# Optimization experiments

Measured on AMD Instinct MI355X. Metric: run time of the kernel, lower is better.

Reference implementation:

```python
import jax, jax.numpy as jnp
import numpy as np

# Module config (from init_kwargs): Occ3D-nuScenes volume
VOL_MIN = np.array([-40.0, -40.0, -1.0], dtype=np.float32)
VOXEL_SIZE = 0.4
GRID_SHAPE = (200, 200, 16)  # (vol_max - vol_min) / voxel_size
K = 6          # fixed per-gaussian window; covers radii <= 0.6m (bbox span <= 5 voxels)
N_GAUSS = 32768
N_DIMS = 16


def setup_inputs() -> dict:
    key = jax.random.key(0)
    k1, k2, k3, k4, k5 = jax.random.split(key, 5)
    # Means strictly inside the volume with 1m margin so bboxes stay in-grid.
    lo = jnp.array([-39.0, -39.0, 0.0], dtype=jnp.float32)
    hi = jnp.array([39.0, 39.0, 4.4], dtype=jnp.float32)
    means3d = jax.random.uniform(k1, (N_GAUSS, 3), minval=lo, maxval=hi, dtype=jnp.float32)
    # SPD covariances: Q diag(s) Q^T with eigenvalues in [0.01, 0.04]
    A = jax.random.normal(k2, (N_GAUSS, 3, 3), dtype=jnp.float32)
    Q, _ = jnp.linalg.qr(A)
    s = jax.random.uniform(k3, (N_GAUSS, 3), minval=0.01, maxval=0.04, dtype=jnp.float32)
    covs = jnp.einsum('nij,nj,nkj->nik', Q, s, Q)
    opacities = jax.random.uniform(k4, (N_GAUSS,), dtype=jnp.float32)
    features = jax.random.normal(k5, (N_GAUSS, N_DIMS), dtype=jnp.float32)
    return {"means3d": means3d, "covs": covs, "opacities": opacities, "features": features}


def reference(means3d, covs, opacities, features):
    N, D = features.shape
    dim_x, dim_y, dim_z = GRID_SHAPE
    total = dim_x * dim_y * dim_z
    vol_min = jnp.asarray(VOL_MIN)

    inv_covs = jnp.linalg.inv(covs)                                  # [N,3,3]
    radii = 3.0 * jnp.sqrt(jnp.diagonal(covs, axis1=-2, axis2=-1))   # [N,3]

    # Bounding box in voxel indices (trunc toward zero, like the triton .to(int32))
    s = (means3d - radii - vol_min) / VOXEL_SIZE
    e = (means3d + radii - vol_min) / VOXEL_SIZE
    start = jnp.maximum(0, s.astype(jnp.int32))                      # [N,3]
    end = jnp.minimum(jnp.array(GRID_SHAPE, jnp.int32), e.astype(jnp.int32) + 1)

    offs = jnp.arange(K, dtype=jnp.int32)
    ix = start[:, 0:1] + offs   # [N,K]
    iy = start[:, 1:2] + offs
    iz = start[:, 2:3] + offs
    mask = ((ix < end[:, 0:1])[:, :, None, None]
            & (iy < end[:, 1:2])[:, None, :, None]
            & (iz < end[:, 2:3])[:, None, None, :])                  # [N,K,K,K]

    # Voxel-corner minus mean offsets (matches kernel: x*vs + vol_min - m)
    px = ix.astype(means3d.dtype) * VOXEL_SIZE + vol_min[0] - means3d[:, 0:1]  # [N,K]
    py = iy.astype(means3d.dtype) * VOXEL_SIZE + vol_min[1] - means3d[:, 1:2]
    pz = iz.astype(means3d.dtype) * VOXEL_SIZE + vol_min[2] - means3d[:, 2:3]
    d = jnp.stack(jnp.broadcast_arrays(px[:, :, None, None],
                                       py[:, None, :, None],
                                       pz[:, None, None, :]), axis=-1)  # [N,K,K,K,3]

    mahal = jnp.einsum('nxyzi,nij,nxyzj->nxyz', d, inv_covs, d)      # [N,K,K,K]
    density = opacities[:, None, None, None] * jnp.exp(-0.5 * mahal)
    density = jnp.where(mask, density, 0.0)

    flat_idx = (ix[:, :, None, None] * (dim_y * dim_z)
                + iy[:, None, :, None] * dim_z
                + iz[:, None, None, :])                               # [N,K,K,K]
    idx = flat_idx.reshape(-1)

    grid_density = jnp.zeros((total,), density.dtype).at[idx].add(density.reshape(-1))

    contrib = density[..., None] * features[:, None, None, None, :]   # [N,K,K,K,D]
    grid_feats = jnp.zeros((total, D), density.dtype).at[:, -1].set(1e-5)
    grid_feats = grid_feats.at[idx].add(contrib.reshape(-1, D))
    grid_feats = grid_feats / jnp.clip(grid_density, 1e-6, None)[:, None]

    return grid_density.reshape(GRID_SHAPE), grid_feats.reshape(*GRID_SHAPE, D)
```

## Files before the change

### kernel.cpp

```cpp
#include <hip/hip_runtime.h>
#include <math.h>

constexpr int   GX = 200, GY = 200, GZ = 16;
constexpr int   TOTAL = GX * GY * GZ;
constexpr int   ND = 16;
constexpr int   KW = 6;
constexpr float VS = 0.4f;
constexpr float VMINX = -40.0f, VMINY = -40.0f, VMINZ = -1.0f;

constexpr int   TS = 4;
constexpr int   TX = 50, TY = 50, TZ = 4;
constexpr int   NT = TX * TY * TZ;
constexpr int   REC = 32;
constexpr int   CAP = 128;
constexpr int   BR  = 8;
constexpr float NHL2E = -0.72134752044448170f;


__global__ __launch_bounds__(256) void gv_prep(
    const float* __restrict__ means, const float* __restrict__ covs,
    const float* __restrict__ opac,  const float* __restrict__ feats,
    float* __restrict__ gdata, int* __restrict__ counts,
    int* __restrict__ entries, int n)
{
    int g = blockIdx.x * 256 + threadIdx.x;
    if (g >= n) return;
    const float* cv = covs + (size_t)g * 9;
    float a = cv[0], b = cv[1], c = cv[2], d = cv[4], e = cv[5], f = cv[8];
    float A = d * f - e * e;
    float B = c * e - b * f;
    float C = b * e - c * d;
    float invdet = 1.0f / (a * A + b * B + c * C);
    float mx = means[g * 3 + 0], my = means[g * 3 + 1], mz = means[g * 3 + 2];
    float rx = 3.0f * sqrtf(a), ry = 3.0f * sqrtf(d), rz = 3.0f * sqrtf(f);
    int sx = max(0, (int)((mx - rx - VMINX) / VS));
    int sy = max(0, (int)((my - ry - VMINY) / VS));
    int sz = max(0, (int)((mz - rz - VMINZ) / VS));
    int ex = min(GX, (int)((mx + rx - VMINX) / VS) + 1); ex = min(ex, sx + KW);
    int ey = min(GY, (int)((my + ry - VMINY) / VS) + 1); ey = min(ey, sy + KW);
    int ez = min(GZ, (int)((mz + rz - VMINZ) / VS) + 1); ez = min(ez, sz + KW);

    float rec[REC];
    rec[0] = mx; rec[1] = my; rec[2] = mz; rec[3] = opac[g];
    rec[4] = (A * invdet) * NHL2E;
    rec[5] = (B * invdet) * (2.0f * NHL2E);
    rec[6] = (C * invdet) * (2.0f * NHL2E);
    rec[7] = ((a * f - c * c) * invdet) * NHL2E;
    rec[8] = ((b * c - a * e) * invdet) * (2.0f * NHL2E);
    rec[9] = ((a * d - b * b) * invdet) * NHL2E;
    rec[10] = __int_as_float(sx | (sy << 8) | (sz << 16));
    rec[11] = __int_as_float(ex | (ey << 8) | (ez << 16));
    rec[12] = 0.0f; rec[13] = 0.0f; rec[14] = 0.0f; rec[15] = 0.0f;
    const float4* f4 = (const float4*)(feats + (size_t)g * ND);
#pragma unroll
    for (int q = 0; q < 4; ++q) {
        float4 v = f4[q];
        rec[16 + q * 4 + 0] = v.x; rec[16 + q * 4 + 1] = v.y;
        rec[16 + q * 4 + 2] = v.z; rec[16 + q * 4 + 3] = v.w;
    }
    float4* dst = (float4*)(gdata + (size_t)g * REC);
#pragma unroll
    for (int q = 0; q < 8; ++q) dst[q] = ((const float4*)rec)[q];

    int tx0 = sx >> 2, tx1 = (ex - 1) >> 2;
    int ty0 = sy >> 2, ty1 = (ey - 1) >> 2;
    int tz0 = sz >> 2, tz1 = (ez - 1) >> 2;
    for (int tx = tx0; tx <= tx1; ++tx)
        for (int ty = ty0; ty <= ty1; ++ty)
            for (int tz = tz0; tz <= tz1; ++tz) {
                int tile = (tx * TY + ty) * TZ + tz;
                int slot = atomicAdd(&counts[tile], 1);
                if (slot < CAP) entries[(size_t)tile * CAP + slot] = g;
            }
}

__global__ __launch_bounds__(256) void gv_tile(
    const float* __restrict__ gdata, const int* __restrict__ counts,
    const int* __restrict__ entries, float* __restrict__ out)
{
    const int blk  = blockIdx.x;
    const int ty   = blk % TY;
    const int tx   = blk / TY;
    const int wv   = threadIdx.x >> 6;
    const int lane = threadIdx.x & 63;
    const int tile = (tx * TY + ty) * TZ + wv;

    __shared__ float sbuf[4][2][BR * REC];

    const int lz = lane & 3, ly = (lane >> 2) & 3, lx = lane >> 4;
    const int ix = tx * TS + lx, iy = ty * TS + ly, iz = wv * TS + lz;
    const float pxc = (float)ix * VS + VMINX;
    const float pyc = (float)iy * VS + VMINY;
    const float pzc = (float)iz * VS + VMINZ;

    float accd = 0.0f;
    float accf[ND];
#pragma unroll
    for (int c = 0; c < ND; ++c) accf[c] = 0.0f;
    accf[ND - 1] = 1e-5f;

    const int cnt = __builtin_amdgcn_readfirstlane(min(counts[tile], CAP));
    const int* __restrict__ el = entries + (size_t)tile * CAP;

    const int rlane = lane >> 3;
    const int flane = lane & 7;
    const int wslot = rlane * REC + flane * 4;

    if (cnt > 0) {
        const int nb = (cnt + BR - 1) >> 3;
        float* b0 = &sbuf[wv][0][0];
        float* b1 = &sbuf[wv][1][0];

        int id0 = el[min(rlane, cnt - 1)];
        float4 v0 = *(const float4*)(gdata + (size_t)id0 * REC + flane * 4);
        *(float4*)(b0 + wslot) = v0;
        int idn = el[min(BR + rlane, cnt - 1)];
        float4 vn = *(const float4*)(gdata + (size_t)idn * REC + flane * 4);
        int idn2 = el[min(2 * BR + rlane, cnt - 1)];

        for (int b = 0; b < nb; ++b) {
            if (b + 1 < nb) {
                float* dst = ((b + 1) & 1) ? b1 : b0;
                *(float4*)(dst + wslot) = vn;
                vn = *(const float4*)(gdata + (size_t)idn2 * REC + flane * 4);
                idn2 = el[min((b + 3) * BR + rlane, cnt - 1)];
            }
            const float* rb = (b & 1) ? b1 : b0;
            const int rn = min(BR, cnt - b * BR);
            for (int r = 0; r < rn; ++r) {
                const float* rec = rb + r * REC;
                float4 q2 = *(const float4*)(rec + 8);
                int spk = __float_as_int(q2.z), epk = __float_as_int(q2.w);
                int sx = spk & 255, sy = (spk >> 8) & 255, sz = (spk >> 16) & 255;
                int ex = epk & 255, ey = (epk >> 8) & 255, ez = (epk >> 16) & 255;
                bool in = (ix >= sx) & (ix < ex)
                        & (iy >= sy) & (iy < ey)
                        & (iz >= sz) & (iz < ez);
                if (__any(in)) {
                    float4 m  = *(const float4*)(rec);
                    float4 q0 = *(const float4*)(rec + 4);
                    float px = pxc - m.x;
                    float py = pyc - m.y;
                    float pz = pzc - m.z;
                    float q = q0.x * px * px + q0.w * py * py + q2.y * pz * pz
                            + q0.y * px * py + q0.z * px * pz + q2.x * py * pz;
                    float dens = m.w * __builtin_amdgcn_exp2f(q);
                    dens = in ? dens : 0.0f;
                    accd += dens;
                    float4 f0 = *(const float4*)(rec + 16);
                    float4 f1 = *(const float4*)(rec + 20);
                    float4 f2 = *(const float4*)(rec + 24);
                    float4 f3 = *(const float4*)(rec + 28);
                    accf[0]  = fmaf(dens, f0.x, accf[0]);
                    accf[1]  = fmaf(dens, f0.y, accf[1]);
                    accf[2]  = fmaf(dens, f0.z, accf[2]);
                    accf[3]  = fmaf(dens, f0.w, accf[3]);
                    accf[4]  = fmaf(dens, f1.x, accf[4]);
                    accf[5]  = fmaf(dens, f1.y, accf[5]);
                    accf[6]  = fmaf(dens, f1.z, accf[6]);
                    accf[7]  = fmaf(dens, f1.w, accf[7]);
                    accf[8]  = fmaf(dens, f2.x, accf[8]);
                    accf[9]  = fmaf(dens, f2.y, accf[9]);
                    accf[10] = fmaf(dens, f2.z, accf[10]);
                    accf[11] = fmaf(dens, f2.w, accf[11]);
                    accf[12] = fmaf(dens, f3.x, accf[12]);
                    accf[13] = fmaf(dens, f3.y, accf[13]);
                    accf[14] = fmaf(dens, f3.z, accf[14]);
                    accf[15] = fmaf(dens, f3.w, accf[15]);
                }
            }
        }
    }

    const int flat = (ix * GY + iy) * GZ + iz;
    out[flat] = accd;
    float inv = 1.0f / fmaxf(accd, 1e-6f);
    float4* fo = (float4*)(out + TOTAL + (size_t)flat * ND);
#pragma unroll
    for (int q = 0; q < 4; ++q) {
        float4 w;
        w.x = accf[q * 4 + 0] * inv;
        w.y = accf[q * 4 + 1] * inv;
        w.z = accf[q * 4 + 2] * inv;
        w.w = accf[q * 4 + 3] * inv;
        fo[q] = w;
    }
}

extern "C" void kernel_launch(void* const* d_in, const int* in_sizes, int n_in,
                              void* d_out, int out_size, void* d_ws, size_t ws_size,
                              hipStream_t stream) {
    const float* means = (const float*)d_in[0];
    const float* covs  = (const float*)d_in[1];
    const float* opac  = (const float*)d_in[2];
    const float* feats = (const float*)d_in[3];
    float* out = (float*)d_out;
    const int n = in_sizes[2];

    float* gdata   = (float*)d_ws;
    int*   counts  = (int*)(gdata + (size_t)n * REC);
    int*   entries = counts + ((NT + 63) & ~63);

    hipMemsetAsync(counts, 0, NT * sizeof(int), stream);
    gv_prep<<<(n + 255) / 256, 256, 0, stream>>>(means, covs, opac, feats,
                                                 gdata, counts, entries, n);
    gv_tile<<<TX * TY, 256, 0, stream>>>(gdata, counts, entries, out);
}
```

Before: 109.4 us.

## Bin gaussians into xy columns and sweep all z-slabs per wave

Gaussians are now binned into 2D xy columns of 4x4 voxels instead of 3D 4x4x4 tiles. Each wave owns one full-height column, and each lane keeps four z-voxel accumulators in registers. The xy part of the quadratic form and the feature loads are computed once per gaussian and reused across z-slabs, and only the slabs the gaussian's z-range overlaps are evaluated. This cuts binning atomics and duplicate record fetches, but it raises register pressure (about 68 accumulators per lane) and launches four times fewer blocks, which may limit occupancy and parallelism.

```diff
diff --git a/kernel.cpp b/kernel.cpp
--- a/kernel.cpp
+++ b/kernel.cpp
@@ -9,8 +9,8 @@
 constexpr float VMINX = -40.0f, VMINY = -40.0f, VMINZ = -1.0f;
 
 constexpr int   TS = 4;
-constexpr int   TX = 50, TY = 50, TZ = 4;
-constexpr int   NT = TX * TY * TZ;
+constexpr int   TX = 50, TY = 50;
+constexpr int   NP = TX * TY;
 constexpr int   REC = 32;
 constexpr int   CAP = 128;
 constexpr int   BR  = 8;
@@ -64,43 +64,50 @@
 
     int tx0 = sx >> 2, tx1 = (ex - 1) >> 2;
     int ty0 = sy >> 2, ty1 = (ey - 1) >> 2;
-    int tz0 = sz >> 2, tz1 = (ez - 1) >> 2;
     for (int tx = tx0; tx <= tx1; ++tx)
-        for (int ty = ty0; ty <= ty1; ++ty)
-            for (int tz = tz0; tz <= tz1; ++tz) {
-                int tile = (tx * TY + ty) * TZ + tz;
-                int slot = atomicAdd(&counts[tile], 1);
-                if (slot < CAP) entries[(size_t)tile * CAP + slot] = g;
-            }
+        for (int ty = ty0; ty <= ty1; ++ty) {
+            int tile = tx * TY + ty;
+            int slot = atomicAdd(&counts[tile], 1);
+            if (slot < CAP) entries[(size_t)tile * CAP + slot] = g;
+        }
 }
 
 __global__ __launch_bounds__(256) void gv_tile(
     const float* __restrict__ gdata, const int* __restrict__ counts,
     const int* __restrict__ entries, float* __restrict__ out)
 {
-    const int blk  = blockIdx.x;
-    const int ty   = blk % TY;
-    const int tx   = blk / TY;
     const int wv   = threadIdx.x >> 6;
     const int lane = threadIdx.x & 63;
-    const int tile = (tx * TY + ty) * TZ + wv;
+    const int p    = blockIdx.x * 4 + wv;
+    const int pty  = p % TY;
+    const int ptx  = p / TY;
 
     __shared__ float sbuf[4][2][BR * REC];
 
-    const int lz = lane & 3, ly = (lane >> 2) & 3, lx = lane >> 4;
-    const int ix = tx * TS + lx, iy = ty * TS + ly, iz = wv * TS + lz;
+    const int lz2 = lane & 3, ly = (lane >> 2) & 3, lx = lane >> 4;
+    const int ix = ptx * TS + lx, iy = pty * TS + ly;
     const float pxc = (float)ix * VS + VMINX;
     const float pyc = (float)iy * VS + VMINY;
-    const float pzc = (float)iz * VS + VMINZ;
-
-    float accd = 0.0f;
-    float accf[ND];
-#pragma unroll
-    for (int c = 0; c < ND; ++c) accf[c] = 0.0f;
-    accf[ND - 1] = 1e-5f;
-
-    const int cnt = __builtin_amdgcn_readfirstlane(min(counts[tile], CAP));
-    const int* __restrict__ el = entries + (size_t)tile * CAP;
+    float pzcv[4];
+    int   izv[4];
+#pragma unroll
+    for (int v = 0; v < 4; ++v) {
+        izv[v] = v * 4 + lz2;
+        pzcv[v] = (float)izv[v] * VS + VMINZ;
+    }
+
+    float accd[4];
+    float accf[4][ND];
+#pragma unroll
+    for (int v = 0; v < 4; ++v) {
+        accd[v] = 0.0f;
+#pragma unroll
+        for (int c = 0; c < ND; ++c) accf[v][c] = 0.0f;
+        accf[v][ND - 1] = 1e-5f;
+    }
+
+    const int cnt = __builtin_amdgcn_readfirstlane(min(counts[p], CAP));
+    const int* __restrict__ el = entries + (size_t)p * CAP;
 
     const int rlane = lane >> 3;
     const int flane = lane & 7;
@@ -133,57 +140,67 @@
                 int spk = __float_as_int(q2.z), epk = __float_as_int(q2.w);
                 int sx = spk & 255, sy = (spk >> 8) & 255, sz = (spk >> 16) & 255;
                 int ex = epk & 255, ey = (epk >> 8) & 255, ez = (epk >> 16) & 255;
-                bool in = (ix >= sx) & (ix < ex)
-                        & (iy >= sy) & (iy < ey)
-                        & (iz >= sz) & (iz < ez);
-                if (__any(in)) {
-                    float4 m  = *(const float4*)(rec);
-                    float4 q0 = *(const float4*)(rec + 4);
-                    float px = pxc - m.x;
-                    float py = pyc - m.y;
-                    float pz = pzc - m.z;
-                    float q = q0.x * px * px + q0.w * py * py + q2.y * pz * pz
-                            + q0.y * px * py + q0.z * px * pz + q2.x * py * pz;
+                bool in_xy = (ix >= sx) & (ix < ex) & (iy >= sy) & (iy < ey);
+
+                float4 m  = *(const float4*)(rec);
+                float4 q0 = *(const float4*)(rec + 4);
+                float px = pxc - m.x;
+                float py = pyc - m.y;
+                float a1 = fmaf(q0.y, py, q0.x * px);
+                float A0 = fmaf(q0.w * py, py, a1 * px);
+                float B0 = fmaf(q2.x, py, q0.z * px);
+
+                float4 f0 = *(const float4*)(rec + 16);
+                float4 f1 = *(const float4*)(rec + 20);
+                float4 f2 = *(const float4*)(rec + 24);
+                float4 f3 = *(const float4*)(rec + 28);
+
+                const int qlo = sz >> 2, qhi = (ez - 1) >> 2;
+#pragma unroll
+                for (int v = 0; v < 4; ++v) {
+                    if (v < qlo || v > qhi) continue;
+                    float pz = pzcv[v] - m.z;
+                    float q = fmaf(pz, fmaf(q2.y, pz, B0), A0);
                     float dens = m.w * __builtin_amdgcn_exp2f(q);
+                    bool in = in_xy & (izv[v] >= sz) & (izv[v] < ez);
                     dens = in ? dens : 0.0f;
-                    accd += dens;
-                    float4 f0 = *(const float4*)(rec + 16);
-                    float4 f1 = *(const float4*)(rec + 20);
-                    float4 f2 = *(const float4*)(rec + 24);
-                    float4 f3 = *(const float4*)(rec + 28);
-                    accf[0]  = fmaf(dens, f0.x, accf[0]);
-                    accf[1]  = fmaf(dens, f0.y, accf[1]);
-                    accf[2]  = fmaf(dens, f0.z, accf[2]);
-                    accf[3]  = fmaf(dens, f0.w, accf[3]);
-                    accf[4]  = fmaf(dens, f1.x, accf[4]);
-                    accf[5]  = fmaf(dens, f1.y, accf[5]);
-                    accf[6]  = fmaf(dens, f1.z, accf[6]);
-                    accf[7]  = fmaf(dens, f1.w, accf[7]);
-                    accf[8]  = fmaf(dens, f2.x, accf[8]);
-                    accf[9]  = fmaf(dens, f2.y, accf[9]);
-                    accf[10] = fmaf(dens, f2.z, accf[10]);
-                    accf[11] = fmaf(dens, f2.w, accf[11]);
-                    accf[12] = fmaf(dens, f3.x, accf[12]);
-                    accf[13] = fmaf(dens, f3.y, accf[13]);
-                    accf[14] = fmaf(dens, f3.z, accf[14]);
-                    accf[15] = fmaf(dens, f3.w, accf[15]);
+                    accd[v] += dens;
+                    accf[v][0]  = fmaf(dens, f0.x, accf[v][0]);
+                    accf[v][1]  = fmaf(dens, f0.y, accf[v][1]);
+                    accf[v][2]  = fmaf(dens, f0.z, accf[v][2]);
+                    accf[v][3]  = fmaf(dens, f0.w, accf[v][3]);
+                    accf[v][4]  = fmaf(dens, f1.x, accf[v][4]);
+                    accf[v][5]  = fmaf(dens, f1.y, accf[v][5]);
+                    accf[v][6]  = fmaf(dens, f1.z, accf[v][6]);
+                    accf[v][7]  = fmaf(dens, f1.w, accf[v][7]);
+                    accf[v][8]  = fmaf(dens, f2.x, accf[v][8]);
+                    accf[v][9]  = fmaf(dens, f2.y, accf[v][9]);
+                    accf[v][10] = fmaf(dens, f2.z, accf[v][10]);
+                    accf[v][11] = fmaf(dens, f2.w, accf[v][11]);
+                    accf[v][12] = fmaf(dens, f3.x, accf[v][12]);
+                    accf[v][13] = fmaf(dens, f3.y, accf[v][13]);
+                    accf[v][14] = fmaf(dens, f3.z, accf[v][14]);
+                    accf[v][15] = fmaf(dens, f3.w, accf[v][15]);
                 }
             }
         }
     }
 
-    const int flat = (ix * GY + iy) * GZ + iz;
-    out[flat] = accd;
-    float inv = 1.0f / fmaxf(accd, 1e-6f);
-    float4* fo = (float4*)(out + TOTAL + (size_t)flat * ND);
-#pragma unroll
-    for (int q = 0; q < 4; ++q) {
-        float4 w;
-        w.x = accf[q * 4 + 0] * inv;
-        w.y = accf[q * 4 + 1] * inv;
-        w.z = accf[q * 4 + 2] * inv;
-        w.w = accf[q * 4 + 3] * inv;
-        fo[q] = w;
+#pragma unroll
+    for (int v = 0; v < 4; ++v) {
+        const int flat = (ix * GY + iy) * GZ + izv[v];
+        out[flat] = accd[v];
+        float inv = 1.0f / fmaxf(accd[v], 1e-6f);
+        float4* fo = (float4*)(out + TOTAL + (size_t)flat * ND);
+#pragma unroll
+        for (int q = 0; q < 4; ++q) {
+            float4 w;
+            w.x = accf[v][q * 4 + 0] * inv;
+            w.y = accf[v][q * 4 + 1] * inv;
+            w.z = accf[v][q * 4 + 2] * inv;
+            w.w = accf[v][q * 4 + 3] * inv;
+            fo[q] = w;
+        }
     }
 }
 
@@ -199,10 +216,10 @@
 
     float* gdata   = (float*)d_ws;
     int*   counts  = (int*)(gdata + (size_t)n * REC);
-    int*   entries = counts + ((NT + 63) & ~63);
-
-    hipMemsetAsync(counts, 0, NT * sizeof(int), stream);
+    int*   entries = counts + ((NP + 63) & ~63);
+
+    hipMemsetAsync(counts, 0, NP * sizeof(int), stream);
     gv_prep<<<(n + 255) / 256, 256, 0, stream>>>(means, covs, opac, feats,
                                                  gdata, counts, entries, n);
-    gv_tile<<<TX * TY, 256, 0, stream>>>(gdata, counts, entries, out);
+    gv_tile<<<NP / 4, 256, 0, stream>>>(gdata, counts, entries, out);
 }
```

Measured after the change: 112.4 us. +2.8%, slower.

## Pack gaussian features as bf16 in compact 20-float records, drop wave skip

Applied to the files above, without the earlier changes.

Stores the per-gaussian features as packed bf16 pairs, which shrinks each staged record from 32 to 20 floats. Batches grow to 12 records per buffer, with 60 lanes staging five float4s each. The per-record __any early-out branch is removed so every record is evaluated unconditionally, and the tile-to-wave mapping changes to a flat linear index. The aim is less gather and LDS traffic and less branch overhead, at the cost of lower feature precision and wasted math on records that hit none of the wave's voxels.

```diff
diff --git a/kernel.cpp b/kernel.cpp
--- a/kernel.cpp
+++ b/kernel.cpp
@@ -11,11 +11,16 @@
 constexpr int   TS = 4;
 constexpr int   TX = 50, TY = 50, TZ = 4;
 constexpr int   NT = TX * TY * TZ;
-constexpr int   REC = 32;
+constexpr int   RS = 20;
 constexpr int   CAP = 128;
-constexpr int   BR  = 8;
+constexpr int   BR  = 12;
 constexpr float NHL2E = -0.72134752044448170f;
 
+
+__device__ __forceinline__ unsigned bf16_rne(float x) {
+    unsigned u = __float_as_uint(x);
+    return (u + 0x7fffu + ((u >> 16) & 1u)) >> 16;
+}
 
 __global__ __launch_bounds__(256) void gv_prep(
     const float* __restrict__ means, const float* __restrict__ covs,
@@ -40,7 +45,7 @@
     int ey = min(GY, (int)((my + ry - VMINY) / VS) + 1); ey = min(ey, sy + KW);
     int ez = min(GZ, (int)((mz + rz - VMINZ) / VS) + 1); ez = min(ez, sz + KW);
 
-    float rec[REC];
+    float rec[RS];
     rec[0] = mx; rec[1] = my; rec[2] = mz; rec[3] = opac[g];
     rec[4] = (A * invdet) * NHL2E;
     rec[5] = (B * invdet) * (2.0f * NHL2E);
@@ -50,17 +55,16 @@
     rec[9] = ((a * d - b * b) * invdet) * NHL2E;
     rec[10] = __int_as_float(sx | (sy << 8) | (sz << 16));
     rec[11] = __int_as_float(ex | (ey << 8) | (ez << 16));
-    rec[12] = 0.0f; rec[13] = 0.0f; rec[14] = 0.0f; rec[15] = 0.0f;
-    const float4* f4 = (const float4*)(feats + (size_t)g * ND);
-#pragma unroll
-    for (int q = 0; q < 4; ++q) {
-        float4 v = f4[q];
-        rec[16 + q * 4 + 0] = v.x; rec[16 + q * 4 + 1] = v.y;
-        rec[16 + q * 4 + 2] = v.z; rec[16 + q * 4 + 3] = v.w;
+    const float* fr = feats + (size_t)g * ND;
+#pragma unroll
+    for (int q = 0; q < 8; ++q) {
+        unsigned lo = bf16_rne(fr[2 * q]);
+        unsigned hi = bf16_rne(fr[2 * q + 1]);
+        rec[12 + q] = __uint_as_float(lo | (hi << 16));
     }
-    float4* dst = (float4*)(gdata + (size_t)g * REC);
-#pragma unroll
-    for (int q = 0; q < 8; ++q) dst[q] = ((const float4*)rec)[q];
+    float4* dst = (float4*)(gdata + (size_t)g * RS);
+#pragma unroll
+    for (int q = 0; q < 5; ++q) dst[q] = ((const float4*)rec)[q];
 
     int tx0 = sx >> 2, tx1 = (ex - 1) >> 2;
     int ty0 = sy >> 2, ty1 = (ey - 1) >> 2;
@@ -78,17 +82,17 @@
     const float* __restrict__ gdata, const int* __restrict__ counts,
     const int* __restrict__ entries, float* __restrict__ out)
 {
-    const int blk  = blockIdx.x;
-    const int ty   = blk % TY;
-    const int tx   = blk / TY;
     const int wv   = threadIdx.x >> 6;
     const int lane = threadIdx.x & 63;
-    const int tile = (tx * TY + ty) * TZ + wv;
-
-    __shared__ float sbuf[4][2][BR * REC];
+    const int p    = blockIdx.x * 4 + wv;
+    const int tz   = p % TZ;
+    const int ty   = (p / TZ) % TY;
+    const int tx   = p / (TZ * TY);
+
+    __shared__ float sbuf[4][2][BR * RS];
 
     const int lz = lane & 3, ly = (lane >> 2) & 3, lx = lane >> 4;
-    const int ix = tx * TS + lx, iy = ty * TS + ly, iz = wv * TS + lz;
+    const int ix = tx * TS + lx, iy = ty * TS + ly, iz = tz * TS + lz;
     const float pxc = (float)ix * VS + VMINX;
     const float pyc = (float)iy * VS + VMINY;
     const float pzc = (float)iz * VS + VMINZ;
@@ -99,75 +103,81 @@
     for (int c = 0; c < ND; ++c) accf[c] = 0.0f;
     accf[ND - 1] = 1e-5f;
 
-    const int cnt = __builtin_amdgcn_readfirstlane(min(counts[tile], CAP));
-    const int* __restrict__ el = entries + (size_t)tile * CAP;
-
-    const int rlane = lane >> 3;
-    const int flane = lane & 7;
-    const int wslot = rlane * REC + flane * 4;
+    const int cnt = __builtin_amdgcn_readfirstlane(min(counts[p], CAP));
+    const int* __restrict__ el = entries + (size_t)p * CAP;
+
+    const int  rl = lane / 5;
+    const int  fc = lane - rl * 5;
+    const bool stager = lane < 60;
+    const int  wslot = rl * RS + fc * 4;
 
     if (cnt > 0) {
-        const int nb = (cnt + BR - 1) >> 3;
+        const int nb = (cnt + BR - 1) / BR;
         float* b0 = &sbuf[wv][0][0];
         float* b1 = &sbuf[wv][1][0];
 
-        int id0 = el[min(rlane, cnt - 1)];
-        float4 v0 = *(const float4*)(gdata + (size_t)id0 * REC + flane * 4);
-        *(float4*)(b0 + wslot) = v0;
-        int idn = el[min(BR + rlane, cnt - 1)];
-        float4 vn = *(const float4*)(gdata + (size_t)idn * REC + flane * 4);
-        int idn2 = el[min(2 * BR + rlane, cnt - 1)];
+        float4 vn; int idn2 = 0;
+        if (stager) {
+            int id0 = el[min(rl, cnt - 1)];
+            float4 v0 = *(const float4*)(gdata + (size_t)id0 * RS + fc * 4);
+            *(float4*)(b0 + wslot) = v0;
+            int idn = el[min(BR + rl, cnt - 1)];
+            vn = *(const float4*)(gdata + (size_t)idn * RS + fc * 4);
+            idn2 = el[min(2 * BR + rl, cnt - 1)];
+        }
 
         for (int b = 0; b < nb; ++b) {
-            if (b + 1 < nb) {
-                float* dst = ((b + 1) & 1) ? b1 : b0;
-                *(float4*)(dst + wslot) = vn;
-                vn = *(const float4*)(gdata + (size_t)idn2 * REC + flane * 4);
-                idn2 = el[min((b + 3) * BR + rlane, cnt - 1)];
+            if (b + 1 < nb && stager) {
+                float* dstb = ((b + 1) & 1) ? b1 : b0;
+                *(float4*)(dstb + wslot) = vn;
+                vn = *(const float4*)(gdata + (size_t)idn2 * RS + fc * 4);
+                idn2 = el[min((b + 3) * BR + rl, cnt - 1)];
             }
             const float* rb = (b & 1) ? b1 : b0;
             const int rn = min(BR, cnt - b * BR);
             for (int r = 0; r < rn; ++r) {
-                const float* rec = rb + r * REC;
-                float4 q2 = *(const float4*)(rec + 8);
-                int spk = __float_as_int(q2.z), epk = __float_as_int(q2.w);
+                const float* rec = rb + r * RS;
+                float4 c2 = *(const float4*)(rec + 8);
+                int spk = __float_as_int(c2.z), epk = __float_as_int(c2.w);
                 int sx = spk & 255, sy = (spk >> 8) & 255, sz = (spk >> 16) & 255;
                 int ex = epk & 255, ey = (epk >> 8) & 255, ez = (epk >> 16) & 255;
                 bool in = (ix >= sx) & (ix < ex)
                         & (iy >= sy) & (iy < ey)
                         & (iz >= sz) & (iz < ez);
-                if (__any(in)) {
-                    float4 m  = *(const float4*)(rec);
-                    float4 q0 = *(const float4*)(rec + 4);
-                    float px = pxc - m.x;
-                    float py = pyc - m.y;
-                    float pz = pzc - m.z;
-                    float q = q0.x * px * px + q0.w * py * py + q2.y * pz * pz
-                            + q0.y * px * py + q0.z * px * pz + q2.x * py * pz;
-                    float dens = m.w * __builtin_amdgcn_exp2f(q);
-                    dens = in ? dens : 0.0f;
-                    accd += dens;
-                    float4 f0 = *(const float4*)(rec + 16);
-                    float4 f1 = *(const float4*)(rec + 20);
-                    float4 f2 = *(const float4*)(rec + 24);
-                    float4 f3 = *(const float4*)(rec + 28);
-                    accf[0]  = fmaf(dens, f0.x, accf[0]);
-                    accf[1]  = fmaf(dens, f0.y, accf[1]);
-                    accf[2]  = fmaf(dens, f0.z, accf[2]);
-                    accf[3]  = fmaf(dens, f0.w, accf[3]);
-                    accf[4]  = fmaf(dens, f1.x, accf[4]);
-                    accf[5]  = fmaf(dens, f1.y, accf[5]);
-                    accf[6]  = fmaf(dens, f1.z, accf[6]);
-                    accf[7]  = fmaf(dens, f1.w, accf[7]);
-                    accf[8]  = fmaf(dens, f2.x, accf[8]);
-                    accf[9]  = fmaf(dens, f2.y, accf[9]);
-                    accf[10] = fmaf(dens, f2.z, accf[10]);
-                    accf[11] = fmaf(dens, f2.w, accf[11]);
-                    accf[12] = fmaf(dens, f3.x, accf[12]);
-                    accf[13] = fmaf(dens, f3.y, accf[13]);
-                    accf[14] = fmaf(dens, f3.z, accf[14]);
-                    accf[15] = fmaf(dens, f3.w, accf[15]);
-                }
+
+                float4 c0 = *(const float4*)(rec);
+                float4 c1 = *(const float4*)(rec + 4);
+                float px = pxc - c0.x;
+                float py = pyc - c0.y;
+                float pz = pzc - c0.z;
+                float q = c1.x * px * px + c1.w * py * py + c2.y * pz * pz
+                        + c1.y * px * py + c1.z * px * pz + c2.x * py * pz;
+                float dens = c0.w * __builtin_amdgcn_exp2f(q);
+                dens = in ? dens : 0.0f;
+                accd += dens;
+
+                uint4 fA = *(const uint4*)(rec + 12);
+                uint4 fB = *(const uint4*)(rec + 16);
+#define BFLO(u) __uint_as_float((u) << 16)
+#define BFHI(u) __uint_as_float((u) & 0xffff0000u)
+                accf[0]  = fmaf(dens, BFLO(fA.x), accf[0]);
+                accf[1]  = fmaf(dens, BFHI(fA.x), accf[1]);
+                accf[2]  = fmaf(dens, BFLO(fA.y), accf[2]);
+                accf[3]  = fmaf(dens, BFHI(fA.y), accf[3]);
+                accf[4]  = fmaf(dens, BFLO(fA.z), accf[4]);
+                accf[5]  = fmaf(dens, BFHI(fA.z), accf[5]);
+                accf[6]  = fmaf(dens, BFLO(fA.w), accf[6]);
+                accf[7]  = fmaf(dens, BFHI(fA.w), accf[7]);
+                accf[8]  = fmaf(dens, BFLO(fB.x), accf[8]);
+                accf[9]  = fmaf(dens, BFHI(fB.x), accf[9]);
+                accf[10] = fmaf(dens, BFLO(fB.y), accf[10]);
+                accf[11] = fmaf(dens, BFHI(fB.y), accf[11]);
+                accf[12] = fmaf(dens, BFLO(fB.z), accf[12]);
+                accf[13] = fmaf(dens, BFHI(fB.z), accf[13]);
+                accf[14] = fmaf(dens, BFLO(fB.w), accf[14]);
+                accf[15] = fmaf(dens, BFHI(fB.w), accf[15]);
+#undef BFLO
+#undef BFHI
             }
         }
     }
@@ -198,11 +208,11 @@
     const int n = in_sizes[2];
 
     float* gdata   = (float*)d_ws;
-    int*   counts  = (int*)(gdata + (size_t)n * REC);
+    int*   counts  = (int*)(gdata + (size_t)n * RS);
     int*   entries = counts + ((NT + 63) & ~63);
 
     hipMemsetAsync(counts, 0, NT * sizeof(int), stream);
     gv_prep<<<(n + 255) / 256, 256, 0, stream>>>(means, covs, opac, feats,
                                                  gdata, counts, entries, n);
-    gv_tile<<<TX * TY, 256, 0, stream>>>(gdata, counts, entries, out);
-}
+    gv_tile<<<NT / 4, 256, 0, stream>>>(gdata, counts, entries, out);
+}
```

New measurement: 106.4 us. -2.7%, faster.
